# Optimization experiments

Hardware: AMD Instinct MI355X
Metric: run time of the kernel (lower is better)

The kernel has to match this reference:

```python
import jax, jax.numpy as jnp
import numpy as np

B, D, SEQ, P0 = 512, 512, 192, 144
P1, P2 = P0 // 3, P0 // 6  # 48, 24


def conv1d(x, w, pad=2):
    # x: [N, C, L], w: [O, C, K]; stride-1 'same' conv (no bias), like nn.Conv1d
    return jax.lax.conv_general_dilated(x, w, window_strides=(1,), padding=[(pad, pad)],
                                        dimension_numbers=('NCH', 'OIH', 'NCH'))


def _dec_layer(x, w):
    # DecoderLayer: x [B, L, C_in] -> elu(conv over channel dim) -> [B, L, C_out]
    return jax.nn.elu(jnp.transpose(conv1d(jnp.transpose(x, (0, 2, 1)), w), (0, 2, 1)))


def _chunk_merge(out, lt, w_a, w_b, step):
    # Vectorized form of the per-chunk loop: fold chunks into batch, one conv call each.
    b, p, d = out.shape
    cnt = p // step
    ya = jax.nn.elu(conv1d(out.reshape(b * cnt, step, d), w_a))   # [b*cnt, step*f, d]
    yb = jax.nn.elu(conv1d(lt.reshape(b * cnt, step, d), w_b))
    f = w_a.shape[0] // step
    return (ya + yb).reshape(b, cnt * step * f, d)


def setup_inputs() -> dict:
    key = jax.random.key(0)
    ks = jax.random.split(key, 19)
    r = lambda i, shp: jax.random.normal(ks[i], shp, dtype=jnp.float32)
    return {
        'enc_out_true': r(0, (B, SEQ // 6, D)),
        'enc_out_pred': r(1, (B, P2, D)),
        'lot0': r(2, (B, SEQ // 3, D)),
        'lot1': r(3, (B, SEQ // 6, D)),
        'lop0': r(4, (B, P1, D)),
        'lop1': r(5, (B, P2, D)),
        'w_conv_z1': r(6, (P2, SEQ // 6, 5)) * 0.05,
        'w_conv_output': r(7, (P2, P2, 5)) * 0.05,
        'w_te0': r(8, (P1, SEQ // 3, 5)) * 0.05,
        'w_te1': r(9, (P2, SEQ // 6, 5)) * 0.05,
        'w_cm0': r(10, (P1, 2 * P1, 5)) * 0.05,
        'w_cm1': r(11, (P2, 2 * P2, 5)) * 0.05,
        'w_m0': r(12, (8, 4, 5)) * 0.05,
        'w_m20': r(13, (8, 4, 5)) * 0.05,
        'w_m1': r(14, (24, 8, 5)) * 0.05,
        'w_m21': r(15, (24, 8, 5)) * 0.05,
        'w_proj': r(16, (7, D, 5)) * 0.05,
        'w_lin': r(17, (P0, P0)) * 0.05,
        'b_lin': r(18, (P0,)) * 0.05,
    }


def reference(enc_out_true, enc_out_pred, lot0, lot1, lop0, lop1,
              w_conv_z1, w_conv_output, w_te0, w_te1, w_cm0, w_cm1,
              w_m0, w_m20, w_m1, w_m21, w_proj, w_lin, b_lin):
    # enc path: conv_z1 then merge with enc_out_pred (dropout is identity at eval)
    et = conv1d(enc_out_true, w_conv_z1)                              # [B, P2, D]
    output = jax.nn.elu(conv1d(enc_out_pred + et, w_conv_output))     # [B, P2, D]

    # ---- layer_len == 1 ----
    lt = _dec_layer(jnp.transpose(lot1, (0, 2, 1)), w_te1)            # [B, D, P2]
    lt = _dec_layer(jnp.concatenate([lt, jnp.transpose(lop1, (0, 2, 1))], axis=-1), w_cm1)  # [B, D, P2]
    output = _chunk_merge(output, jnp.transpose(lt, (0, 2, 1)), w_m0, w_m20, 4)             # [B, P1, D]

    # ---- layer_len == 0 ----
    lt = _dec_layer(jnp.transpose(lot0, (0, 2, 1)), w_te0)            # [B, D, P1]
    lt = _dec_layer(jnp.concatenate([lt, jnp.transpose(lop0, (0, 2, 1))], axis=-1), w_cm0)  # [B, D, P1]
    output = _chunk_merge(output, jnp.transpose(lt, (0, 2, 1)), w_m1, w_m21, 8)             # [B, P0, D]

    # projection conv with circular padding over length P0
    x = jnp.transpose(output, (0, 2, 1))                              # [B, D, P0]
    x = jnp.pad(x, ((0, 0), (0, 0), (2, 2)), mode='wrap')
    proj = conv1d(x, w_proj, pad=0)                                   # [B, c_out, P0]
    # Linear(P0, P0) applied along the length axis
    y = jnp.einsum('bcp,op->bco', proj, w_lin) + b_lin                # [B, c_out, P0]
    return jnp.transpose(y, (0, 2, 1))                                # [B, P0, c_out]
```

## Files before the change

kernel.cpp:

```cpp
#include <hip/hip_runtime.h>
#include <hip/hip_bf16.h>


typedef _Float16 h16;
typedef _Float16 h16x8 __attribute__((ext_vector_type(8)));
typedef _Float16 h16x4 __attribute__((ext_vector_type(4)));
typedef float    f32x4 __attribute__((ext_vector_type(4)));

#define MFMA16(a,b,c) __builtin_amdgcn_mfma_f32_16x16x32_f16((a),(b),(c),0,0,0)

__device__ __forceinline__ int clampi(int x, int lo, int hi){ return x < lo ? lo : (x > hi ? hi : x); }
__device__ __forceinline__ float eluf(float v){ return v > 0.f ? v : (__expf(v) - 1.f); }

#define S40  40
#define S56  56
#define S72  72
#define S104 104
#define SO2  136

enum {
  OFF_WZ1  = 0,
  OFF_WOUT = 5120,
  OFF_WTE1 = 10240,
  OFF_WCM1 = 15360,
  OFF_WTE0 = 25600,
  OFF_WCM0 = 40960,
  OFF_WM0  = 64000,
  OFF_WM20 = 64512,
  OFF_WM1  = 65024,
  OFF_WM21 = 67072,
  OFF_WP   = 69120,
  PACKED_TOTAL = 93696
};

__global__ void pack_weights(const float* wz1, const float* wout, const float* wte1,
    const float* wcm1, const float* wte0, const float* wcm0,
    const float* wm0, const float* wm20, const float* wm1, const float* wm21,
    const float* wproj, h16* wp)
{
  const int t = threadIdx.x;
  auto packBig = [&](const float* src, int O, int C, h16* dst, int Opad, int Cpad){
    const int n = Opad*5*Cpad;
    for (int i = t; i < n; i += blockDim.x){
      int c = i % Cpad; int k = (i / Cpad) % 5; int o = i / (Cpad*5);
      float v = (o < O && c < C) ? src[(o*C + c)*5 + k] : 0.f;
      dst[i] = (h16)v;
    }
  };
  switch (blockIdx.x){
    case 0: packBig(wz1, 24, 32, wp+OFF_WZ1, 32, 32); break;
    case 1: packBig(wout, 24, 24, wp+OFF_WOUT, 32, 32); break;
    case 2: packBig(wte1, 24, 32, wp+OFF_WTE1, 32, 32); break;
    case 3: packBig(wcm1, 24, 48, wp+OFF_WCM1, 32, 64); break;
    case 4: packBig(wte0, 48, 64, wp+OFF_WTE0, 48, 64); break;
    case 5: packBig(wcm0, 48, 96, wp+OFF_WCM0, 48, 96); break;
    case 6: {
      for (int i = t; i < 512; i += blockDim.x){
        int q = i & 31, o = i >> 5; float v = 0.f;
        if (o < 8 && q < 20){ int k = q >> 2, c = q & 3; v = wm0[(o*4 + c)*5 + k]; }
        wp[OFF_WM0 + i] = (h16)v;
      }
      for (int i = t; i < 512; i += blockDim.x){
        int q = i & 31, o = i >> 5; float v = 0.f;
        if (o < 8 && q < 20){ int k = q >> 2, c = q & 3; v = wm20[(o*4 + c)*5 + k]; }
        wp[OFF_WM20 + i] = (h16)v;
      }
    } break;
    case 7: {
      for (int i = t; i < 2048; i += blockDim.x){
        int q = i & 63, o = i >> 6; float v = 0.f;
        if (o < 24 && q < 40){ int k = q >> 3, c = q & 7; v = wm1[(o*8 + c)*5 + k]; }
        wp[OFF_WM1 + i] = (h16)v;
      }
      for (int i = t; i < 2048; i += blockDim.x){
        int q = i & 63, o = i >> 6; float v = 0.f;
        if (o < 24 && q < 40){ int k = q >> 3, c = q & 7; v = wm21[(o*8 + c)*5 + k]; }
        wp[OFF_WM21 + i] = (h16)v;
      }
    } break;
    case 8: {
      for (int i = t; i < 48*512; i += blockDim.x){
        int d = i & 511, r = i >> 9; float v = 0.f;
        if (r < 35){ int jj = r / 5, k = r - jj*5; v = wproj[(jj*512 + d)*5 + k]; }
        wp[OFF_WP + i] = (h16)v;
      }
    } break;
  }
}


__device__ __forceinline__ void loadT(const float* __restrict__ src, int C, int CB16,
    h16* __restrict__ XT, int S, int co, int d0, int wave, int lane)
{
  const int m = lane & 15, q = lane >> 4;
  const int UNITS = CB16*9;
  for (int u = wave; u < UNITS; u += 8){
    const int cb = u / 9, db = u - cb*9;
    const int row = db*16 + m;
    const int dg = d0 - 8 + row;
    const bool dok = ((unsigned)dg < 512u);
    const int cbase = cb*16 + q*4;
    h16x4 pk;
    #pragma unroll
    for (int i = 0; i < 4; ++i){
      const int c = cbase + i;
      float v = (dok && c < C) ? src[c*512 + dg] : 0.f;
      pk[i] = (h16)v;
    }
    *(h16x4*)(XT + row*S + co + cbase) = pk;
  }
}

__device__ __forceinline__ void zeroCols(h16* XT, int S, int c0, int nc, int tid){
  for (int i = tid; i < 144*nc; i += 512){
    const int r = i / nc, c = i - r*nc;
    XT[r*S + c0 + c] = (h16)0.f;
  }
}

template<int CB, int EPI>
__device__ __forceinline__ void convGemm(const h16* __restrict__ XT, int S,
    const h16* __restrict__ Wp, h16* __restrict__ XTo, int So, int co,
    int OT, int Oreal, int d0, int wave, int lane)
{
  const int m = lane & 15, kg = lane >> 4;
  const int Cpad = CB*32;
  const int NT = OT*9;
  h16x8 B[5][CB];
  int otPrev = -1;
  for (int tix = wave; tix < NT; tix += 8){
    const int ot = tix / 9, rt = tix - ot*9;
    if (ot != otPrev){
      otPrev = ot;
      const int o = ot*16 + m;
      const h16* wb = Wp + o*5*Cpad + kg*8;
      #pragma unroll
      for (int k = 0; k < 5; ++k)
        #pragma unroll
        for (int cb = 0; cb < CB; ++cb)
          B[k][cb] = *(const h16x8*)(wb + k*Cpad + cb*32);
    }
    f32x4 acc = {0.f,0.f,0.f,0.f};
    const int rbase = rt*16 + m - 2;
    #pragma unroll
    for (int k = 0; k < 5; ++k){
      const int r = clampi(rbase + k, 0, 143);
      const h16* ap = XT + r*S + kg*8;
      #pragma unroll
      for (int cb = 0; cb < CB; ++cb)
        acc = MFMA16(*(const h16x8*)(ap + cb*32), B[k][cb], acc);
    }
    const int o = ot*16 + m;
    if (o < Oreal){
      #pragma unroll
      for (int r4 = 0; r4 < 4; ++r4){
        const int row = rt*16 + kg*4 + r4;
        const bool dz = ((unsigned)(d0 - 8 + row) < 512u);
        float v = acc[r4];
        h16* p = XTo + row*So + co + o;
        if (EPI == 0) *p = dz ? (h16)((float)(*p) + v) : (h16)0.f;
        else          *p = dz ? (h16)eluf(v)           : (h16)0.f;
      }
    }
  }
}

__device__ __forceinline__ void chunk4(const h16* __restrict__ out0, const h16* __restrict__ lt1,
    const h16* __restrict__ wA, const h16* __restrict__ wB, h16* __restrict__ out1,
    int d0, int wave, int lane)
{
  const int m = lane & 15, kg = lane >> 4;
  const h16x8 bA = *(const h16x8*)(wA + m*32 + kg*8);
  const h16x8 bB = *(const h16x8*)(wB + m*32 + kg*8);
  for (int tix = wave; tix < 54; tix += 8){
    const int j = tix / 9, rt = tix - j*9;
    const int rb = rt*16 + m;
    const int r0 = clampi(rb + 2*kg - 2, 0, 143);
    const int r1 = clampi(rb + 2*kg - 1, 0, 143);
    h16x4 lo = *(const h16x4*)(out0 + r0*S40 + 4*j);
    h16x4 hi = *(const h16x4*)(out0 + r1*S40 + 4*j);
    h16x8 a = __builtin_shufflevector(lo, hi, 0,1,2,3,4,5,6,7);
    f32x4 accA = {0.f,0.f,0.f,0.f};
    accA = MFMA16(a, bA, accA);
    lo = *(const h16x4*)(lt1 + r0*S40 + 4*j);
    hi = *(const h16x4*)(lt1 + r1*S40 + 4*j);
    a = __builtin_shufflevector(lo, hi, 0,1,2,3,4,5,6,7);
    f32x4 accB = {0.f,0.f,0.f,0.f};
    accB = MFMA16(a, bB, accB);
    if (m < 8){
      #pragma unroll
      for (int r4 = 0; r4 < 4; ++r4){
        const int row = rt*16 + kg*4 + r4;
        const bool dz = ((unsigned)(d0 - 8 + row) < 512u);
        out1[row*S56 + 8*j + m] = dz ? (h16)(eluf(accA[r4]) + eluf(accB[r4])) : (h16)0.f;
      }
    }
  }
}

__device__ __forceinline__ void chunk8(const h16* __restrict__ out1, const h16* __restrict__ lt0,
    const h16* __restrict__ wA, const h16* __restrict__ wB, h16* __restrict__ o2t,
    int j, int wave, int lane)
{
  const int m = lane & 15, kg = lane >> 4;
  for (int tix = wave; tix < 16; tix += 8){
    const int ot = tix >> 3, rt = tix & 7;
    const int o = ot*16 + m;
    const h16x8 bA0 = *(const h16x8*)(wA + o*64 + kg*8);
    const h16x8 bA1 = *(const h16x8*)(wA + o*64 + 32 + kg*8);
    const h16x8 bB0 = *(const h16x8*)(wB + o*64 + kg*8);
    const h16x8 bB1 = *(const h16x8*)(wB + o*64 + 32 + kg*8);
    const int rb = rt*16 + m + 8;
    const int rA0 = rb + kg - 2;
    const int rA1 = clampi(rb + kg + 2, 0, 143);
    h16x8 a0 = *(const h16x8*)(out1 + rA0*S56 + 8*j);
    h16x8 a1 = *(const h16x8*)(out1 + rA1*S56 + 8*j);
    f32x4 accA = {0.f,0.f,0.f,0.f};
    accA = MFMA16(a0, bA0, accA);
    accA = MFMA16(a1, bA1, accA);
    a0 = *(const h16x8*)(lt0 + rA0*S56 + 8*j);
    a1 = *(const h16x8*)(lt0 + rA1*S56 + 8*j);
    f32x4 accB = {0.f,0.f,0.f,0.f};
    accB = MFMA16(a0, bB0, accB);
    accB = MFMA16(a1, bB1, accB);
    h16x4 pk;
    #pragma unroll
    for (int r4 = 0; r4 < 4; ++r4)
      pk[r4] = (h16)(eluf(accA[r4]) + eluf(accB[r4]));
    *(h16x4*)(o2t + o*SO2 + rt*16 + kg*4) = pk;
  }
}

__device__ __forceinline__ void projAcc(const h16* __restrict__ WPp, const h16* __restrict__ o2t,
    float* __restrict__ PROJ, int j, int d0, int wave, int lane)
{
  const int m = lane & 15, kg = lane >> 4;
  for (int tix = wave; tix < 6; tix += 8){
    const int ct = tix & 1, rt = tix >> 1;
    f32x4 acc = {0.f,0.f,0.f,0.f};
    const h16* ap = WPp + (rt*16 + m)*512 + d0 + kg*8;
    const h16* bp = o2t + (ct*16 + m)*SO2 + kg*8;
    #pragma unroll
    for (int ks = 0; ks < 4; ++ks)
      acc = MFMA16(*(const h16x8*)(ap + ks*32), *(const h16x8*)(bp + ks*32), acc);
    const int pl = ct*16 + m;
    if (pl < 24){
      #pragma unroll
      for (int r4 = 0; r4 < 4; ++r4){
        const int rowm = rt*16 + kg*4 + r4;
        if (rowm < 35) PROJ[rowm*144 + j*24 + pl] += acc[r4];
      }
    }
  }
}

__global__ __launch_bounds__(512, 2) void decoder_fused(
    const float* __restrict__ enc_true, const float* __restrict__ enc_pred,
    const float* __restrict__ lot0, const float* __restrict__ lot1,
    const float* __restrict__ lop0, const float* __restrict__ lop1,
    const h16* __restrict__ wp, const float* __restrict__ w_lin,
    const float* __restrict__ b_lin, float* __restrict__ out)
{
  __shared__ __align__(16) char smem[110144];
  float* PROJ = (float*)smem;
  h16* B1 = (h16*)(smem + 20160);
  h16* B2 = (h16*)(smem + 50112);
  h16* B3 = (h16*)(smem + 70848);
  h16* B4 = (h16*)(smem + 82368);
  h16* B5 = (h16*)(smem + 93888);

  const int b = blockIdx.x;
  const int tid = threadIdx.x;
  const int wave = tid >> 6, lane = tid & 63;

  const float* p_true = enc_true + (size_t)b*32*512;
  const float* p_pred = enc_pred + (size_t)b*24*512;
  const float* p_lot1 = lot1 + (size_t)b*32*512;
  const float* p_lop1 = lop1 + (size_t)b*24*512;
  const float* p_lot0 = lot0 + (size_t)b*64*512;
  const float* p_lop0 = lop0 + (size_t)b*48*512;

  for (int i = tid; i < 35*144; i += 512) PROJ[i] = 0.f;
  __syncthreads();

  for (int t = 0; t < 4; ++t){
    const int d0 = t*128;

    loadT(p_true, 32, 2, B2, S40, 0, d0, wave, lane);
    loadT(p_pred, 24, 2, B1, S40, 0, d0, wave, lane);
    __syncthreads();

    convGemm<1,0>(B2, S40, wp+OFF_WZ1, B1, S40, 0, 2, 24, d0, wave, lane);
    __syncthreads();

    convGemm<1,1>(B1, S40, wp+OFF_WOUT, B3, S40, 0, 2, 24, d0, wave, lane);
    loadT(p_lot1, 32, 2, B2, S40, 0, d0, wave, lane);
    __syncthreads();

    convGemm<1,1>(B2, S40, wp+OFF_WTE1, B1, S72, 0, 2, 24, d0, wave, lane);
    loadT(p_lop1, 24, 2, B1, S72, 24, d0, wave, lane);
    zeroCols(B1, S72, 56, 8, tid);
    __syncthreads();

    convGemm<2,1>(B1, S72, wp+OFF_WCM1, B4, S40, 0, 2, 24, d0, wave, lane);
    loadT(p_lot0, 64, 4, B2, S72, 0, d0, wave, lane);
    __syncthreads();

    chunk4(B3, B4, wp+OFF_WM0, wp+OFF_WM20, B5, d0, wave, lane);
    __syncthreads();

    convGemm<2,1>(B2, S72, wp+OFF_WTE0, B1, S104, 0, 3, 48, d0, wave, lane);
    loadT(p_lop0, 48, 3, B1, S104, 48, d0, wave, lane);
    __syncthreads();

    convGemm<3,1>(B1, S104, wp+OFF_WCM0, B2, S56, 0, 3, 48, d0, wave, lane);
    __syncthreads();

    for (int j = 0; j < 6; ++j){
      chunk8(B5, B2, wp+OFF_WM1, wp+OFF_WM21, B3, j, wave, lane);
      __syncthreads();
      projAcc(wp+OFF_WP, B3, PROJ, j, d0, wave, lane);
      __syncthreads();
    }
  }

  float* projF = (float*)B4;
  for (int i = tid; i < 7*144; i += 512){
    const int jj = i / 144, p = i - jj*144;
    float s = 0.f;
    #pragma unroll
    for (int k = 0; k < 5; ++k){
      int pp = p + k - 2; pp = (pp + 144) % 144;
      s += PROJ[(jj*5 + k)*144 + pp];
    }
    projF[i] = s;
  }
  __syncthreads();
  for (int i = tid; i < 1008; i += 512){
    const int o = i / 7, jj = i - o*7;
    float acc = b_lin[o];
    const float* wl = w_lin + o*144;
    const float* pr = (const float*)projF + jj*144;
    for (int p = 0; p < 144; ++p) acc += pr[p] * wl[p];
    out[(size_t)b*1008 + i] = acc;
  }
}

extern "C" void kernel_launch(void* const* d_in, const int* in_sizes, int n_in,
                              void* d_out, int out_size, void* d_ws, size_t ws_size,
                              hipStream_t stream)
{
  if (ws_size < (size_t)PACKED_TOTAL * sizeof(h16)) return;
  h16* wp = (h16*)d_ws;
  pack_weights<<<9, 256, 0, stream>>>(
      (const float*)d_in[6],
      (const float*)d_in[7],
      (const float*)d_in[9],
      (const float*)d_in[11],
      (const float*)d_in[8],
      (const float*)d_in[10],
      (const float*)d_in[12],
      (const float*)d_in[13],
      (const float*)d_in[14],
      (const float*)d_in[15],
      (const float*)d_in[16],
      wp);
  decoder_fused<<<512, 512, 0, stream>>>(
      (const float*)d_in[0], (const float*)d_in[1],
      (const float*)d_in[2], (const float*)d_in[3],
      (const float*)d_in[4], (const float*)d_in[5],
      wp, (const float*)d_in[17], (const float*)d_in[18],
      (float*)d_out);
}
```

Before: 846.9 us.

## Halve feature-tile width to cut LDS and double-buffer chunk8 output

Shrinks the per-iteration D tile from 128 to 64 columns (80 rows with halo instead of 144), which roughly cuts shared memory from 110KB to 79KB, and raises launch bounds to request more resident blocks. The chunk8 output is ping-ponged between two buffers so one barrier per j-iteration can be removed. The cost is twice as many outer iterations with a larger relative halo overhead (16 of 80 rows) and more barriers overall. Whether 79KB actually allows more than one 512-thread block per CU, and how the tighter register budget affects spills, determines the outcome.

```diff
diff --git a/kernel.cpp b/kernel.cpp
--- a/kernel.cpp
+++ b/kernel.cpp
@@ -16,7 +16,10 @@
 #define S56  56
 #define S72  72
 #define S104 104
-#define SO2  136
+#define SO2  72
+
+#define ROWS 80
+#define RT5  5
 
 enum {
   OFF_WZ1  = 0,
@@ -93,9 +96,9 @@
     h16* __restrict__ XT, int S, int co, int d0, int wave, int lane)
 {
   const int m = lane & 15, q = lane >> 4;
-  const int UNITS = CB16*9;
+  const int UNITS = CB16*RT5;
   for (int u = wave; u < UNITS; u += 8){
-    const int cb = u / 9, db = u - cb*9;
+    const int cb = u / RT5, db = u - cb*RT5;
     const int row = db*16 + m;
     const int dg = d0 - 8 + row;
     const bool dok = ((unsigned)dg < 512u);
@@ -112,7 +115,7 @@
 }
 
 __device__ __forceinline__ void zeroCols(h16* XT, int S, int c0, int nc, int tid){
-  for (int i = tid; i < 144*nc; i += 512){
+  for (int i = tid; i < ROWS*nc; i += 512){
     const int r = i / nc, c = i - r*nc;
     XT[r*S + c0 + c] = (h16)0.f;
   }
@@ -125,11 +128,11 @@
 {
   const int m = lane & 15, kg = lane >> 4;
   const int Cpad = CB*32;
-  const int NT = OT*9;
+  const int NT = OT*RT5;
   h16x8 B[5][CB];
   int otPrev = -1;
   for (int tix = wave; tix < NT; tix += 8){
-    const int ot = tix / 9, rt = tix - ot*9;
+    const int ot = tix / RT5, rt = tix - ot*RT5;
     if (ot != otPrev){
       otPrev = ot;
       const int o = ot*16 + m;
@@ -144,7 +147,7 @@
     const int rbase = rt*16 + m - 2;
     #pragma unroll
     for (int k = 0; k < 5; ++k){
-      const int r = clampi(rbase + k, 0, 143);
+      const int r = clampi(rbase + k, 0, ROWS-1);
       const h16* ap = XT + r*S + kg*8;
       #pragma unroll
       for (int cb = 0; cb < CB; ++cb)
@@ -172,11 +175,11 @@
   const int m = lane & 15, kg = lane >> 4;
   const h16x8 bA = *(const h16x8*)(wA + m*32 + kg*8);
   const h16x8 bB = *(const h16x8*)(wB + m*32 + kg*8);
-  for (int tix = wave; tix < 54; tix += 8){
-    const int j = tix / 9, rt = tix - j*9;
+  for (int tix = wave; tix < 6*RT5; tix += 8){
+    const int j = tix / RT5, rt = tix - j*RT5;
     const int rb = rt*16 + m;
-    const int r0 = clampi(rb + 2*kg - 2, 0, 143);
-    const int r1 = clampi(rb + 2*kg - 1, 0, 143);
+    const int r0 = clampi(rb + 2*kg - 2, 0, ROWS-1);
+    const int r1 = clampi(rb + 2*kg - 1, 0, ROWS-1);
     h16x4 lo = *(const h16x4*)(out0 + r0*S40 + 4*j);
     h16x4 hi = *(const h16x4*)(out0 + r1*S40 + 4*j);
     h16x8 a = __builtin_shufflevector(lo, hi, 0,1,2,3,4,5,6,7);
@@ -203,8 +206,8 @@
     int j, int wave, int lane)
 {
   const int m = lane & 15, kg = lane >> 4;
-  for (int tix = wave; tix < 16; tix += 8){
-    const int ot = tix >> 3, rt = tix & 7;
+  for (int tix = wave; tix < 8; tix += 8){
+    const int ot = tix >> 2, rt = tix & 3;
     const int o = ot*16 + m;
     const h16x8 bA0 = *(const h16x8*)(wA + o*64 + kg*8);
     const h16x8 bA1 = *(const h16x8*)(wA + o*64 + 32 + kg*8);
@@ -212,7 +215,7 @@
     const h16x8 bB1 = *(const h16x8*)(wB + o*64 + 32 + kg*8);
     const int rb = rt*16 + m + 8;
     const int rA0 = rb + kg - 2;
-    const int rA1 = clampi(rb + kg + 2, 0, 143);
+    const int rA1 = clampi(rb + kg + 2, 0, ROWS-1);
     h16x8 a0 = *(const h16x8*)(out1 + rA0*S56 + 8*j);
     h16x8 a1 = *(const h16x8*)(out1 + rA1*S56 + 8*j);
     f32x4 accA = {0.f,0.f,0.f,0.f};
@@ -241,7 +244,7 @@
     const h16* ap = WPp + (rt*16 + m)*512 + d0 + kg*8;
     const h16* bp = o2t + (ct*16 + m)*SO2 + kg*8;
     #pragma unroll
-    for (int ks = 0; ks < 4; ++ks)
+    for (int ks = 0; ks < 2; ++ks)
       acc = MFMA16(*(const h16x8*)(ap + ks*32), *(const h16x8*)(bp + ks*32), acc);
     const int pl = ct*16 + m;
     if (pl < 24){
@@ -254,20 +257,22 @@
   }
 }
 
-__global__ __launch_bounds__(512, 2) void decoder_fused(
+__global__ __launch_bounds__(512, 4) void decoder_fused(
     const float* __restrict__ enc_true, const float* __restrict__ enc_pred,
     const float* __restrict__ lot0, const float* __restrict__ lot1,
     const float* __restrict__ lop0, const float* __restrict__ lop1,
     const h16* __restrict__ wp, const float* __restrict__ w_lin,
     const float* __restrict__ b_lin, float* __restrict__ out)
 {
-  __shared__ __align__(16) char smem[110144];
+  __shared__ __align__(16) char smem[79296];
   float* PROJ = (float*)smem;
   h16* B1 = (h16*)(smem + 20160);
-  h16* B2 = (h16*)(smem + 50112);
-  h16* B3 = (h16*)(smem + 70848);
-  h16* B4 = (h16*)(smem + 82368);
-  h16* B5 = (h16*)(smem + 93888);
+  h16* B2 = (h16*)(smem + 36800);
+  h16* B3 = (h16*)(smem + 48320);
+  h16* B4 = (h16*)(smem + 54720);
+  h16* B5 = (h16*)(smem + 61120);
+  h16* O2a = (h16*)(smem + 70080);
+  h16* O2b = (h16*)(smem + 74688);
 
   const int b = blockIdx.x;
   const int tid = threadIdx.x;
@@ -283,8 +288,8 @@
   for (int i = tid; i < 35*144; i += 512) PROJ[i] = 0.f;
   __syncthreads();
 
-  for (int t = 0; t < 4; ++t){
-    const int d0 = t*128;
+  for (int t = 0; t < 8; ++t){
+    const int d0 = t*64;
 
     loadT(p_true, 32, 2, B2, S40, 0, d0, wave, lane);
     loadT(p_pred, 24, 2, B1, S40, 0, d0, wave, lane);
@@ -317,12 +322,13 @@
     __syncthreads();
 
     for (int j = 0; j < 6; ++j){
-      chunk8(B5, B2, wp+OFF_WM1, wp+OFF_WM21, B3, j, wave, lane);
+      h16* o2 = (j & 1) ? O2b : O2a;
+      chunk8(B5, B2, wp+OFF_WM1, wp+OFF_WM21, o2, j, wave, lane);
       __syncthreads();
-      projAcc(wp+OFF_WP, B3, PROJ, j, d0, wave, lane);
-      __syncthreads();
-    }
-  }
+      projAcc(wp+OFF_WP, o2, PROJ, j, d0, wave, lane);
+    }
+  }
+  __syncthreads();
 
   float* projF = (float*)B4;
   for (int i = tid; i < 7*144; i += 512){
```

New measurement: 734.2 us. 13.3% less time.
